# Optimization experiments

Hardware: AMD Instinct MI355X
Metric: run time of the kernel (lower is better)

## Reference

```python
import jax, jax.numpy as jnp
import numpy as np


def setup_inputs() -> dict:
    key = jax.random.key(0)
    x = jax.random.normal(key, (1024, 65536), dtype=jnp.float32)
    return {"input": x}


def reference(input) -> jnp.ndarray:
    B = input.shape[0]
    flat = input.reshape(B, -1)            # [B, N]
    N = flat.shape[1]
    idx = int(N * 0.8)                      # 80th-percentile position (ascending sort)
    cutoff = jnp.sort(flat, axis=-1)[:, idx]  # [B]
    cutoff = jax.lax.stop_gradient(cutoff)
    # broadcast cutoff back over all non-batch dims
    cutoff = cutoff.reshape((B,) + (1,) * (input.ndim - 1))
    return jax.nn.relu(input - cutoff)
```

## Files before the change

kernel.cpp:

```cpp
#include <hip/hip_runtime.h>


#define TPB1  512
#define NB    2048
#define CAP   6144
#define TINY  64
#define BLO   0.72f
#define BHI   0.98f

#define TPB2  256
#define VPT   16

__device__ __forceinline__ unsigned f2ord(float f) {
    unsigned u = __float_as_uint(f);
    return (u & 0x80000000u) ? ~u : (u | 0x80000000u);
}
__device__ __forceinline__ float ord2f(unsigned u) {
    unsigned b = (u & 0x80000000u) ? (u ^ 0x80000000u) : ~u;
    return __uint_as_float(b);
}

__device__ __forceinline__ void hist_select(const unsigned* hist, unsigned r, int tid,
                                            unsigned* wsum, unsigned* wbase,
                                            int* s_bin, unsigned* s_cum) {
    const int lane = tid & 63, wid = tid >> 6;
    const int b0 = tid * (NB / TPB1);
    unsigned h0 = hist[b0], h1 = hist[b0+1], h2 = hist[b0+2], h3 = hist[b0+3];
    unsigned s = h0 + h1 + h2 + h3;
    unsigned incl = s;
    #pragma unroll
    for (int off = 1; off < 64; off <<= 1) {
        unsigned t = __shfl_up(incl, off);
        if (lane >= off) incl += t;
    }
    if (lane == 63) wsum[wid] = incl;
    __syncthreads();
    if (tid == 0) {
        unsigned c = 0;
        #pragma unroll
        for (int w = 0; w < TPB1/64; ++w) { wbase[w] = c; c += wsum[w]; }
    }
    __syncthreads();
    unsigned excl = wbase[wid] + incl - s;
    if (r >= excl && r < excl + s) {
        unsigned c = excl;
        if (r < c + h0)        { *s_bin = b0;     *s_cum = c; }
        else { c += h0; if (r < c + h1) { *s_bin = b0 + 1; *s_cum = c; }
        else { c += h1; if (r < c + h2) { *s_bin = b0 + 2; *s_cum = c; }
        else { c += h2;                   *s_bin = b0 + 3; *s_cum = c; } } }
    }
    __syncthreads();
}

__global__ __launch_bounds__(TPB1, 8)
void cutoff_kernel(const float* __restrict__ in, float* __restrict__ cut,
                   int N, int k) {
    const int row  = blockIdx.x;
    const int tid  = threadIdx.x;
    const int lane = tid & 63;
    const int nv   = N >> 2;
    const float SCALE = (float)NB / (BHI - BLO);
    const float4* __restrict__ rowv = (const float4*)(in + (size_t)row * (size_t)N);

    __shared__ unsigned hist[NB];
    __shared__ unsigned cand[CAP];
    __shared__ unsigned tiny[TINY];
    __shared__ unsigned wsum[TPB1/64], wbase[TPB1/64];
    __shared__ unsigned s_cnt, s_below, s_cum, s_tc;
    __shared__ int s_bin, s_fb;
    __shared__ float s_cut;

    for (int i = tid; i < NB; i += TPB1) hist[i] = 0u;
    if (tid == 0) { s_cnt = 0u; s_below = 0u; s_tc = 0u; s_fb = 0; }
    __syncthreads();

    unsigned below = 0;
    for (int i = tid; i < nv; i += TPB1) {
        float4 v = rowv[i];
        float vals[4] = {v.x, v.y, v.z, v.w};
        #pragma unroll
        for (int j = 0; j < 4; ++j) {
            float f = vals[j];
            below += (f < BLO) ? 1u : 0u;
            if (f >= BLO && f < BHI) {
                unsigned p = atomicAdd(&s_cnt, 1u);
                if (p < CAP) cand[p] = __float_as_uint(f);
            }
        }
    }
    #pragma unroll
    for (int o = 32; o > 0; o >>= 1) below += __shfl_down(below, o);
    if (lane == 0) atomicAdd(&s_below, below);
    __syncthreads();

    const unsigned M0 = s_cnt;
    const long long r2ll = (long long)k - (long long)s_below;
    const bool fast = (M0 <= CAP) && (r2ll >= 0) && (r2ll < (long long)M0);

    if (fast) {
        const unsigned r2 = (unsigned)r2ll;
        for (unsigned i = tid; i < M0; i += TPB1) {
            float f = __uint_as_float(cand[i]);
            int b = (int)((f - BLO) * SCALE);
            b = b < 0 ? 0 : (b >= NB ? NB - 1 : b);
            atomicAdd(&hist[b], 1u);
        }
        __syncthreads();
        hist_select(hist, r2, tid, wsum, wbase, &s_bin, &s_cum);
        const int bin = s_bin;
        const unsigned r3 = r2 - s_cum;
        for (unsigned i = tid; i < M0; i += TPB1) {
            unsigned u = cand[i];
            float f = __uint_as_float(u);
            int b = (int)((f - BLO) * SCALE);
            b = b < 0 ? 0 : (b >= NB ? NB - 1 : b);
            if (b == bin) { unsigned p = atomicAdd(&s_tc, 1u); if (p < TINY) tiny[p] = u; }
        }
        __syncthreads();
        const unsigned c = s_tc;
        if (c > TINY) { if (tid == 0) s_fb = 1; }
        else if (tid < 64) {
            unsigned uj = (lane < (int)c) ? tiny[lane] : 0xFFFFFFFFu;
            unsigned less = 0, eq = 0;
            for (unsigned i2 = 0; i2 < c; ++i2) {
                unsigned ui = tiny[i2];
                less += (ui < uj) ? 1u : 0u;
                eq   += (ui == uj) ? 1u : 0u;
            }
            bool cond = (lane < (int)c) && (less <= r3) && (r3 < less + eq);
            unsigned long long cm = __ballot(cond);
            if (cond && lane == __ffsll((long long)cm) - 1)
                s_cut = __uint_as_float(uj);
        }
    } else {
        if (tid == 0) s_fb = 1;
    }
    __syncthreads();

    if (s_fb) {
        unsigned prefix = 0;
        unsigned rr = (unsigned)k;
        const int shifts[3] = {21, 10, 0};
        const int bitsc[3]  = {11, 11, 10};
        for (int pass = 0; pass < 3; ++pass) {
            const int sh = shifts[pass];
            const unsigned nb = 1u << bitsc[pass];
            for (int i = tid; i < NB; i += TPB1) hist[i] = 0u;
            __syncthreads();
            for (int i = tid; i < nv; i += TPB1) {
                float4 v = rowv[i];
                float vals[4] = {v.x, v.y, v.z, v.w};
                #pragma unroll
                for (int j = 0; j < 4; ++j) {
                    unsigned u = f2ord(vals[j]);
                    if (pass == 0 || (u >> (sh + bitsc[pass])) == prefix)
                        atomicAdd(&hist[(u >> sh) & (nb - 1u)], 1u);
                }
            }
            __syncthreads();
            hist_select(hist, rr, tid, wsum, wbase, &s_bin, &s_cum);
            prefix = (prefix << bitsc[pass]) | (unsigned)s_bin;
            rr -= s_cum;
            __syncthreads();
        }
        if (tid == 0) s_cut = ord2f(prefix);
        __syncthreads();
    }

    if (tid == 0) cut[row] = s_cut;
}

__global__ __launch_bounds__(TPB2)
void relu_kernel(const float* __restrict__ in, const float* __restrict__ cut,
                 float* __restrict__ out, int N) {
    const int f4PerBlock = TPB2 * VPT;
    const int bpr = (N >> 2) / f4PerBlock;
    const int row = blockIdx.x / bpr;
    const float c = cut[row];
    const size_t base = (size_t)blockIdx.x * (size_t)f4PerBlock + threadIdx.x;
    const float4* __restrict__ iv = (const float4*)in;
    float4* __restrict__ ov = (float4*)out;
    #pragma unroll
    for (int j = 0; j < VPT; ++j) {
        size_t idx = base + (size_t)j * TPB2;
        float4 v = iv[idx];
        float4 o;
        o.x = fmaxf(v.x - c, 0.0f);
        o.y = fmaxf(v.y - c, 0.0f);
        o.z = fmaxf(v.z - c, 0.0f);
        o.w = fmaxf(v.w - c, 0.0f);
        ov[idx] = o;
    }
}

extern "C" void kernel_launch(void* const* d_in, const int* in_sizes, int n_in,
                              void* d_out, int out_size, void* d_ws, size_t ws_size,
                              hipStream_t stream) {
    const float* in = (const float*)d_in[0];
    float* out = (float*)d_out;
    float* cut = (float*)d_ws;
    const int N = 65536;
    const int B = in_sizes[0] / N;
    const int k = (int)(((long long)N * 4) / 5);

    cutoff_kernel<<<dim3(B), dim3(TPB1), 0, stream>>>(in, cut, N, k);

    const int totalF4 = (B * N) >> 2;
    const int blocks2 = totalF4 / (TPB2 * VPT);
    relu_kernel<<<dim3(blocks2), dim3(TPB2), 0, stream>>>(in, cut, out, N);
}
```

Measured before the change: 488.9 us.

## Fuse cutoff selection and shifted ReLU into one register-resident kernel

Merges the per-row cutoff kernel and the elementwise ReLU kernel into a single kernel. Each thread keeps its 32 float4 values of the row in registers, so the row is read from global memory once instead of twice, and the second launch and the workspace round trip go away. The fallback radix passes also reuse the register copy instead of rereading global memory. In exchange the kernel needs 128 floats of registers per thread, which lowers occupancy, and the write of each row must wait until that row's selection finishes.

```diff
diff --git a/kernel.cpp b/kernel.cpp
--- a/kernel.cpp
+++ b/kernel.cpp
@@ -1,15 +1,13 @@
 #include <hip/hip_runtime.h>
 
 
-#define TPB1  512
+#define TPB   512
+#define F4PT  32
 #define NB    2048
 #define CAP   6144
 #define TINY  64
 #define BLO   0.72f
 #define BHI   0.98f
-
-#define TPB2  256
-#define VPT   16
 
 __device__ __forceinline__ unsigned f2ord(float f) {
     unsigned u = __float_as_uint(f);
@@ -24,7 +22,7 @@
                                             unsigned* wsum, unsigned* wbase,
                                             int* s_bin, unsigned* s_cum) {
     const int lane = tid & 63, wid = tid >> 6;
-    const int b0 = tid * (NB / TPB1);
+    const int b0 = tid * (NB / TPB);
     unsigned h0 = hist[b0], h1 = hist[b0+1], h2 = hist[b0+2], h3 = hist[b0+3];
     unsigned s = h0 + h1 + h2 + h3;
     unsigned incl = s;
@@ -38,7 +36,7 @@
     if (tid == 0) {
         unsigned c = 0;
         #pragma unroll
-        for (int w = 0; w < TPB1/64; ++w) { wbase[w] = c; c += wsum[w]; }
+        for (int w = 0; w < TPB/64; ++w) { wbase[w] = c; c += wsum[w]; }
     }
     __syncthreads();
     unsigned excl = wbase[wid] + incl - s;
@@ -52,41 +50,44 @@
     __syncthreads();
 }
 
-__global__ __launch_bounds__(TPB1, 8)
-void cutoff_kernel(const float* __restrict__ in, float* __restrict__ cut,
-                   int N, int k) {
+__global__ __launch_bounds__(TPB)
+void xsrelu_fused(const float* __restrict__ in, float* __restrict__ out,
+                  int N, int k) {
     const int row  = blockIdx.x;
     const int tid  = threadIdx.x;
     const int lane = tid & 63;
-    const int nv   = N >> 2;
     const float SCALE = (float)NB / (BHI - BLO);
     const float4* __restrict__ rowv = (const float4*)(in + (size_t)row * (size_t)N);
+    float4* __restrict__ outv = (float4*)(out + (size_t)row * (size_t)N);
 
     __shared__ unsigned hist[NB];
     __shared__ unsigned cand[CAP];
     __shared__ unsigned tiny[TINY];
-    __shared__ unsigned wsum[TPB1/64], wbase[TPB1/64];
+    __shared__ unsigned wsum[TPB/64], wbase[TPB/64];
     __shared__ unsigned s_cnt, s_below, s_cum, s_tc;
     __shared__ int s_bin, s_fb;
     __shared__ float s_cut;
 
-    for (int i = tid; i < NB; i += TPB1) hist[i] = 0u;
+    for (int i = tid; i < NB; i += TPB) hist[i] = 0u;
     if (tid == 0) { s_cnt = 0u; s_below = 0u; s_tc = 0u; s_fb = 0; }
     __syncthreads();
 
+    float4 v[F4PT];
+    #pragma unroll
+    for (int j = 0; j < F4PT; ++j) v[j] = rowv[tid + j * TPB];
+
     unsigned below = 0;
-    for (int i = tid; i < nv; i += TPB1) {
-        float4 v = rowv[i];
-        float vals[4] = {v.x, v.y, v.z, v.w};
-        #pragma unroll
-        for (int j = 0; j < 4; ++j) {
-            float f = vals[j];
-            below += (f < BLO) ? 1u : 0u;
-            if (f >= BLO && f < BHI) {
-                unsigned p = atomicAdd(&s_cnt, 1u);
-                if (p < CAP) cand[p] = __float_as_uint(f);
-            }
-        }
+    #pragma unroll
+    for (int j = 0; j < F4PT; ++j) {
+        const float f0 = v[j].x, f1 = v[j].y, f2 = v[j].z, f3 = v[j].w;
+        below += (f0 < BLO) ? 1u : 0u;
+        below += (f1 < BLO) ? 1u : 0u;
+        below += (f2 < BLO) ? 1u : 0u;
+        below += (f3 < BLO) ? 1u : 0u;
+        if (f0 >= BLO && f0 < BHI) { unsigned p = atomicAdd(&s_cnt, 1u); if (p < CAP) cand[p] = __float_as_uint(f0); }
+        if (f1 >= BLO && f1 < BHI) { unsigned p = atomicAdd(&s_cnt, 1u); if (p < CAP) cand[p] = __float_as_uint(f1); }
+        if (f2 >= BLO && f2 < BHI) { unsigned p = atomicAdd(&s_cnt, 1u); if (p < CAP) cand[p] = __float_as_uint(f2); }
+        if (f3 >= BLO && f3 < BHI) { unsigned p = atomicAdd(&s_cnt, 1u); if (p < CAP) cand[p] = __float_as_uint(f3); }
     }
     #pragma unroll
     for (int o = 32; o > 0; o >>= 1) below += __shfl_down(below, o);
@@ -99,7 +100,7 @@
 
     if (fast) {
         const unsigned r2 = (unsigned)r2ll;
-        for (unsigned i = tid; i < M0; i += TPB1) {
+        for (unsigned i = tid; i < M0; i += TPB) {
             float f = __uint_as_float(cand[i]);
             int b = (int)((f - BLO) * SCALE);
             b = b < 0 ? 0 : (b >= NB ? NB - 1 : b);
@@ -109,7 +110,7 @@
         hist_select(hist, r2, tid, wsum, wbase, &s_bin, &s_cum);
         const int bin = s_bin;
         const unsigned r3 = r2 - s_cum;
-        for (unsigned i = tid; i < M0; i += TPB1) {
+        for (unsigned i = tid; i < M0; i += TPB) {
             unsigned u = cand[i];
             float f = __uint_as_float(u);
             int b = (int)((f - BLO) * SCALE);
@@ -144,52 +145,38 @@
         const int bitsc[3]  = {11, 11, 10};
         for (int pass = 0; pass < 3; ++pass) {
             const int sh = shifts[pass];
-            const unsigned nb = 1u << bitsc[pass];
-            for (int i = tid; i < NB; i += TPB1) hist[i] = 0u;
+            const unsigned nbm = (1u << bitsc[pass]) - 1u;
+            for (int i = tid; i < NB; i += TPB) hist[i] = 0u;
             __syncthreads();
-            for (int i = tid; i < nv; i += TPB1) {
-                float4 v = rowv[i];
-                float vals[4] = {v.x, v.y, v.z, v.w};
+            #pragma unroll
+            for (int j = 0; j < F4PT; ++j) {
+                const float vals[4] = {v[j].x, v[j].y, v[j].z, v[j].w};
                 #pragma unroll
-                for (int j = 0; j < 4; ++j) {
-                    unsigned u = f2ord(vals[j]);
+                for (int q = 0; q < 4; ++q) {
+                    unsigned u = f2ord(vals[q]);
                     if (pass == 0 || (u >> (sh + bitsc[pass])) == prefix)
-                        atomicAdd(&hist[(u >> sh) & (nb - 1u)], 1u);
+                        atomicAdd(&hist[(u >> sh) & nbm], 1u);
                 }
             }
             __syncthreads();
             hist_select(hist, rr, tid, wsum, wbase, &s_bin, &s_cum);
             prefix = (prefix << bitsc[pass]) | (unsigned)s_bin;
             rr -= s_cum;
-            __syncthreads();
         }
         if (tid == 0) s_cut = ord2f(prefix);
         __syncthreads();
     }
 
-    if (tid == 0) cut[row] = s_cut;
-}
+    const float cut = s_cut;
 
-__global__ __launch_bounds__(TPB2)
-void relu_kernel(const float* __restrict__ in, const float* __restrict__ cut,
-                 float* __restrict__ out, int N) {
-    const int f4PerBlock = TPB2 * VPT;
-    const int bpr = (N >> 2) / f4PerBlock;
-    const int row = blockIdx.x / bpr;
-    const float c = cut[row];
-    const size_t base = (size_t)blockIdx.x * (size_t)f4PerBlock + threadIdx.x;
-    const float4* __restrict__ iv = (const float4*)in;
-    float4* __restrict__ ov = (float4*)out;
     #pragma unroll
-    for (int j = 0; j < VPT; ++j) {
-        size_t idx = base + (size_t)j * TPB2;
-        float4 v = iv[idx];
+    for (int j = 0; j < F4PT; ++j) {
         float4 o;
-        o.x = fmaxf(v.x - c, 0.0f);
-        o.y = fmaxf(v.y - c, 0.0f);
-        o.z = fmaxf(v.z - c, 0.0f);
-        o.w = fmaxf(v.w - c, 0.0f);
-        ov[idx] = o;
+        o.x = fmaxf(v[j].x - cut, 0.0f);
+        o.y = fmaxf(v[j].y - cut, 0.0f);
+        o.z = fmaxf(v[j].z - cut, 0.0f);
+        o.w = fmaxf(v[j].w - cut, 0.0f);
+        outv[tid + j * TPB] = o;
     }
 }
 
@@ -198,14 +185,9 @@
                               hipStream_t stream) {
     const float* in = (const float*)d_in[0];
     float* out = (float*)d_out;
-    float* cut = (float*)d_ws;
     const int N = 65536;
     const int B = in_sizes[0] / N;
     const int k = (int)(((long long)N * 4) / 5);
 
-    cutoff_kernel<<<dim3(B), dim3(TPB1), 0, stream>>>(in, cut, N, k);
-
-    const int totalF4 = (B * N) >> 2;
-    const int blocks2 = totalF4 / (TPB2 * VPT);
-    relu_kernel<<<dim3(blocks2), dim3(TPB2), 0, stream>>>(in, cut, out, N);
+    xsrelu_fused<<<dim3(B), dim3(TPB), 0, stream>>>(in, out, N, k);
 }
```

New measurement: 475.0 us. -2.8%, faster.
